# Kernel tuning notes

Measured on AMD Instinct MI355X. Metric: run time of the kernel, lower is better.

Reference implementation:

```python
import jax, jax.numpy as jnp
import numpy as np

NEG_SLOPE = 0.2
EPS = 1e-16


def gat_layer(x, src, dst, W, att_src, att_dst, bias, heads, out_ch, concat, n_nodes):
    # Linear projection -> [N, H, C]
    h = (x @ W).reshape(n_nodes, heads, out_ch)
    # Per-node attention logits [N, H]
    a_src = (h * att_src[None]).sum(-1)
    a_dst = (h * att_dst[None]).sum(-1)
    # Per-edge logits, LeakyReLU (message j -> i with src=j, dst=i)
    alpha = a_src[src] + a_dst[dst]                      # [E, H]
    alpha = jnp.where(alpha >= 0, alpha, NEG_SLOPE * alpha)
    # Segment softmax over incoming edges of each dst node
    amax = jax.ops.segment_max(alpha, dst, num_segments=n_nodes)  # [N, H]
    ealpha = jnp.exp(alpha - amax[dst])
    denom = jax.ops.segment_sum(ealpha, dst, num_segments=n_nodes)
    alpha = ealpha / (denom[dst] + EPS)
    # Weighted messages + scatter-add aggregation
    msg = h[src] * alpha[..., None]                      # [E, H, C]
    out = jax.ops.segment_sum(msg, dst, num_segments=n_nodes)  # [N, H, C]
    out = out.reshape(n_nodes, heads * out_ch) if concat else out.mean(axis=1)
    return out + bias


def setup_inputs() -> dict:
    key = jax.random.key(0)
    ks = jax.random.split(key, 11)
    N, E, F, H, C1 = 50000, 1600000, 128, 8, 8
    x = jax.random.normal(ks[0], (N, F), dtype=jnp.float32)
    edge_index = jax.random.randint(ks[1], (2, E), 0, N, dtype=jnp.int64)
    s = 1.0 / np.sqrt(F)
    W1 = jax.random.normal(ks[2], (F, H * C1), dtype=jnp.float32) * s
    att_src1 = jax.random.normal(ks[3], (H, C1), dtype=jnp.float32) * 0.1
    att_dst1 = jax.random.normal(ks[4], (H, C1), dtype=jnp.float32) * 0.1
    bias1 = jax.random.normal(ks[5], (H * C1,), dtype=jnp.float32) * 0.1
    W2 = jax.random.normal(ks[6], (H * C1, F), dtype=jnp.float32) * (1.0 / np.sqrt(H * C1))
    att_src2 = jax.random.normal(ks[7], (1, F), dtype=jnp.float32) * 0.1
    att_dst2 = jax.random.normal(ks[8], (1, F), dtype=jnp.float32) * 0.1
    bias2 = jax.random.normal(ks[9], (F,), dtype=jnp.float32) * 0.1
    return {"x": x, "edge_index": edge_index, "W1": W1, "att_src1": att_src1,
            "att_dst1": att_dst1, "bias1": bias1, "W2": W2, "att_src2": att_src2,
            "att_dst2": att_dst2, "bias2": bias2}


def reference(x, edge_index, W1, att_src1, att_dst1, bias1, W2, att_src2, att_dst2, bias2):
    N = x.shape[0]
    # PyG GATConv add_self_loops=True: append (i, i) for every node
    loops = jnp.arange(N, dtype=edge_index.dtype)
    src = jnp.concatenate([edge_index[0], loops])
    dst = jnp.concatenate([edge_index[1], loops])
    # eval mode: dropouts are identity
    h = gat_layer(x, src, dst, W1, att_src1, att_dst1, bias1, heads=8, out_ch=8,
                  concat=True, n_nodes=N)            # [N, 64]
    h = jax.nn.elu(h)
    out = gat_layer(h, src, dst, W2, att_src2, att_dst2, bias2, heads=1, out_ch=128,
                    concat=False, n_nodes=N)         # [N, 128]
    return out
```

## Files before the change

### kernel.cpp

```cpp
#include <hip/hip_runtime.h>
#include <stdint.h>

#define NEG_SLOPE 0.2f
#define EPSV 1e-16f
#define NBLK 256

typedef __attribute__((ext_vector_type(8))) short short8;
typedef __attribute__((ext_vector_type(4))) float f32x4;

__device__ inline short bf16r(float f){
  union { float f; unsigned u; } v; v.f = f;
  unsigned r = (v.u + 0x7FFFu + ((v.u >> 16) & 1u)) >> 16;
  return (short)r;
}
__device__ inline float bf16lo(unsigned u){
  union { unsigned u; float f; } v; v.u = u << 16; return v.f;
}
__device__ inline float bf16hi(unsigned u){
  union { unsigned u; float f; } v; v.u = u & 0xFFFF0000u; return v.f;
}

__device__ inline void get_edge(const void* ei, int is64, int E, int e, int& s, int& d){
  if (e >= E){ s = d = e - E; return; }
  if (is64){
    const long long* p = (const long long*)ei;
    s = (int)p[e]; d = (int)p[(long long)E + e];
  } else {
    const int* p = (const int*)ei;
    s = p[e]; d = p[E + e];
  }
}

__device__ inline int get_dst(const void* ei, int is64, int E, int e){
  if (e >= E) return e - E;
  if (is64) return (int)((const long long*)ei)[(long long)E + e];
  return ((const int*)ei)[E + e];
}

__global__ void detect_dtype(const int* ei32, int* flag){
  if (threadIdx.x == 0 && blockIdx.x == 0){
    int nz = 0;
    for (int i = 0; i < 64; ++i) nz |= ei32[2*i + 1];
    *flag = (nz == 0) ? 1 : 0;
  }
}

__global__ void cvt_to_bf16(const float* __restrict__ x, short* __restrict__ xb, int n4){
  int i = blockIdx.x*blockDim.x + threadIdx.x;
  if (i >= n4) return;
  f32x4 v = *(const f32x4*)(x + (size_t)i*4);
  short4 o;
  o.x = bf16r(v[0]); o.y = bf16r(v[1]); o.z = bf16r(v[2]); o.w = bf16r(v[3]);
  *(short4*)(xb + (size_t)i*4) = o;
}

__device__ inline void pack_one(const float* W, short* Wp, int NCOL, int idx){
  int NNT = NCOL >> 4;
  int j = idx & 7, n16 = (idx >> 3) & 15, q = (idx >> 7) & 3, tile = idx >> 9;
  int nt = tile % NNT, kt = tile / NNT;
  int k = kt*32 + q*8 + j, n = nt*16 + n16;
  Wp[idx] = bf16r(W[k*NCOL + n]);
}
__global__ void pack_w_both(const float* __restrict__ W1, short* __restrict__ W1p,
                            const float* __restrict__ W2, short* __restrict__ W2p){
  int idx = blockIdx.x*blockDim.x + threadIdx.x;
  if (idx < 8192) pack_one(W1, W1p, 64, idx);
  else            pack_one(W2, W2p, 128, idx - 8192);
}

template<int K, int NCOL>
__global__ __launch_bounds__(256) void gemm_mfma(const short* __restrict__ A, const short* __restrict__ Bp,
                                                 short* __restrict__ Cb, int M){
  constexpr int NKT = K/32, NNT = NCOL/16;
  int wave = (blockIdx.x*256 + (int)threadIdx.x) >> 6;
  int lane = threadIdx.x & 63;
  int row0 = wave << 4;
  if (row0 >= M) return;
  int m = lane & 15, q = lane >> 4;
  f32x4 acc[NNT];
#pragma unroll
  for (int i = 0; i < NNT; ++i) acc[i] = (f32x4){0.f,0.f,0.f,0.f};
#pragma unroll
  for (int kt = 0; kt < NKT; ++kt){
    short8 a = *(const short8*)(A + (size_t)(row0 + m)*K + kt*32 + q*8);
#pragma unroll
    for (int nt = 0; nt < NNT; ++nt){
      short8 b = *(const short8*)(Bp + (size_t)(((kt*NNT + nt)*4 + q)*16 + m)*8);
      acc[nt] = __builtin_amdgcn_mfma_f32_16x16x32_bf16(a, b, acc[nt], 0, 0, 0);
    }
  }
#pragma unroll
  for (int nt = 0; nt < NNT; ++nt){
#pragma unroll
    for (int r = 0; r < 4; ++r){
      Cb[(size_t)(row0 + q*4 + r)*NCOL + nt*16 + m] = bf16r(acc[nt][r]);
    }
  }
}

__global__ void logits_l1(const unsigned short* __restrict__ h1b, const float* __restrict__ att_s,
                          const float* __restrict__ att_d, float* __restrict__ asrc,
                          float* __restrict__ adst, int N){
  int tid = threadIdx.x;
  int n = blockIdx.x*4 + (tid >> 6);
  int j = tid & 63;
  if (n >= N) return;
  float h = bf16lo((unsigned)h1b[(size_t)n*64 + j]);
  float ps = h * att_s[j];
  float pd = h * att_d[j];
#pragma unroll
  for (int mm = 4; mm; mm >>= 1){ ps += __shfl_xor(ps, mm, 8); pd += __shfl_xor(pd, mm, 8); }
  if ((j & 7) == 0){ asrc[n*8 + (j >> 3)] = ps; adst[n*8 + (j >> 3)] = pd; }
}

__global__ void logits_l2(const unsigned* __restrict__ h2u, const float* __restrict__ att_s,
                          const float* __restrict__ att_d, float* __restrict__ asrc,
                          float* __restrict__ adst, int N){
  int tid = threadIdx.x;
  int n = blockIdx.x*4 + (tid >> 6);
  int l = tid & 63;
  if (n >= N) return;
  unsigned u = h2u[(size_t)n*64 + l];
  float x0 = bf16lo(u), x1 = bf16hi(u);
  float ps = x0*att_s[2*l] + x1*att_s[2*l + 1];
  float pd = x0*att_d[2*l] + x1*att_d[2*l + 1];
#pragma unroll
  for (int mm = 32; mm; mm >>= 1){ ps += __shfl_xor(ps, mm, 64); pd += __shfl_xor(pd, mm, 64); }
  if (l == 0){ asrc[n] = ps; adst[n] = pd; }
}

__global__ __launch_bounds__(256) void p1_hist(const void* ei, const int* flag, int E, int E2,
                                               int* __restrict__ block_counts){
  __shared__ int h[256];
  int t = threadIdx.x, blk = blockIdx.x;
  h[t] = 0; __syncthreads();
  int chunk = (E2 + NBLK - 1)/NBLK;
  int beg = blk*chunk, end = min(beg + chunk, E2);
  int is64 = *flag;
  for (int e = beg + t; e < end; e += 256){
    int d = get_dst(ei, is64, E, e);
    atomicAdd(&h[d >> 8], 1);
  }
  __syncthreads();
  block_counts[blk*256 + t] = h[t];
}

__global__ void p2_bucket_scan(const int* __restrict__ block_counts, int* __restrict__ bucket_base){
  __shared__ int sd[256];
  int t = threadIdx.x;
  int tot = 0;
  for (int b = 0; b < NBLK; ++b) tot += block_counts[b*256 + t];
  sd[t] = tot; __syncthreads();
  for (int off = 1; off < 256; off <<= 1){
    int v = (t >= off) ? sd[t - off] : 0;
    __syncthreads(); sd[t] += v; __syncthreads();
  }
  bucket_base[t] = sd[t] - tot;
  if (t == 255) bucket_base[256] = sd[255];
}

__global__ void p2_block_off(const int* __restrict__ block_counts, const int* __restrict__ bucket_base,
                             int* __restrict__ block_off){
  __shared__ int sd[256];
  int b = blockIdx.x, t = threadIdx.x;
  int v = block_counts[t*256 + b];
  sd[t] = v; __syncthreads();
  for (int off = 1; off < 256; off <<= 1){
    int u = (t >= off) ? sd[t - off] : 0;
    __syncthreads(); sd[t] += u; __syncthreads();
  }
  block_off[t*256 + b] = bucket_base[b] + sd[t] - v;
}

__global__ __launch_bounds__(256) void p3_scatter(const void* ei, const int* flag, int E, int E2,
                                                  const int* __restrict__ block_off,
                                                  unsigned* __restrict__ packed){
  __shared__ int cur[256];
  int t = threadIdx.x, blk = blockIdx.x;
  cur[t] = block_off[blk*256 + t];
  __syncthreads();
  int chunk = (E2 + NBLK - 1)/NBLK;
  int beg = blk*chunk, end = min(beg + chunk, E2);
  int is64 = *flag;
  for (int e = beg + t; e < end; e += 256){
    int s, d; get_edge(ei, is64, E, e, s, d);
    int pos = atomicAdd(&cur[d >> 8], 1);
    packed[pos] = ((unsigned)s << 8) | (unsigned)(d & 255);
  }
}

__global__ __launch_bounds__(256) void p4_sort(const unsigned* __restrict__ packed,
                                               const int* __restrict__ bucket_base,
                                               int N, int E2,
                                               int* __restrict__ offs, int* __restrict__ srcs){
  __shared__ int hist[256];
  __shared__ int cur[256];
  int b = blockIdx.x, t = threadIdx.x;
  int base = bucket_base[b], cnt = bucket_base[b + 1] - base;
  hist[t] = 0; __syncthreads();
  for (int p = t; p < cnt; p += 256){
    atomicAdd(&hist[packed[base + p] & 255u], 1);
  }
  __syncthreads();
  int v = hist[t];
  cur[t] = v; __syncthreads();
  for (int off = 1; off < 256; off <<= 1){
    int u = (t >= off) ? cur[t - off] : 0;
    __syncthreads(); cur[t] += u; __syncthreads();
  }
  int ex = cur[t] - v;
  __syncthreads();
  cur[t] = ex;
  int node = b*256 + t;
  if (node < N) offs[node] = base + ex;
  __syncthreads();
  for (int p = t; p < cnt; p += 256){
    unsigned pk = packed[base + p];
    int pos = atomicAdd(&cur[pk & 255u], 1);
    srcs[base + pos] = (int)(pk >> 8);
  }
  if (b == 0 && t == 0) offs[N] = E2;
}

__global__ __launch_bounds__(256) void agg_l1(const char* __restrict__ h1b,
                       const float* __restrict__ asrc, const float* __restrict__ adst,
                       const int* __restrict__ offs, const int* __restrict__ srcs,
                       const float* __restrict__ bias, uint4* __restrict__ hout, int N){
  int tid = threadIdx.x;
  int i = blockIdx.x*4 + (tid >> 6);
  if (i >= N) return;
  int lane = tid & 63, g = lane >> 3, c = lane & 7;
  float ad = adst[i*8 + c];
  int beg = offs[i], end = offs[i + 1], last = end - 1;
  float acc[8];
#pragma unroll
  for (int k = 0; k < 8; ++k) acc[k] = 0.f;
  float den = 0.f;
  for (int p = beg; p < end; p += 32){
    int m[4], s[4];
#pragma unroll
    for (int k = 0; k < 4; ++k) m[k] = p + 8*k + g;
#pragma unroll
    for (int k = 0; k < 4; ++k) s[k] = srcs[min(m[k], last)];
    float a[4];
#pragma unroll
    for (int k = 0; k < 4; ++k) a[k] = asrc[s[k]*8 + c];
    uint4 v[4];
#pragma unroll
    for (int k = 0; k < 4; ++k) v[k] = *(const uint4*)(h1b + ((size_t)s[k] << 7) + (c << 4));
    float w[4];
#pragma unroll
    for (int k = 0; k < 4; ++k){
      float z = a[k] + ad; z = (z >= 0.f) ? z : NEG_SLOPE*z;
      w[k] = (m[k] < end) ? __expf(z) : 0.f;
      den += w[k];
    }
#pragma unroll
    for (int k = 0; k < 4; ++k){
      acc[0] = fmaf(w[k], bf16lo(v[k].x), acc[0]); acc[1] = fmaf(w[k], bf16hi(v[k].x), acc[1]);
      acc[2] = fmaf(w[k], bf16lo(v[k].y), acc[2]); acc[3] = fmaf(w[k], bf16hi(v[k].y), acc[3]);
      acc[4] = fmaf(w[k], bf16lo(v[k].z), acc[4]); acc[5] = fmaf(w[k], bf16hi(v[k].z), acc[5]);
      acc[6] = fmaf(w[k], bf16lo(v[k].w), acc[6]); acc[7] = fmaf(w[k], bf16hi(v[k].w), acc[7]);
    }
  }
#pragma unroll
  for (int mm = 8; mm <= 32; mm <<= 1){
#pragma unroll
    for (int k = 0; k < 8; ++k) acc[k] += __shfl_xor(acc[k], mm, 64);
    den += __shfl_xor(den, mm, 64);
  }
  if (g == 0){
    float inv = 1.f/(den + EPSV);
    unsigned pk[4];
#pragma unroll
    for (int k = 0; k < 4; ++k){
      float o0 = acc[2*k]*inv     + bias[c*8 + 2*k];
      float o1 = acc[2*k + 1]*inv + bias[c*8 + 2*k + 1];
      o0 = (o0 > 0.f) ? o0 : (__expf(o0) - 1.f);
      o1 = (o1 > 0.f) ? o1 : (__expf(o1) - 1.f);
      pk[k] = (unsigned)(unsigned short)bf16r(o0) | ((unsigned)(unsigned short)bf16r(o1) << 16);
    }
    uint4 o; o.x = pk[0]; o.y = pk[1]; o.z = pk[2]; o.w = pk[3];
    hout[(size_t)i*8 + c] = o;
  }
}

__global__ __launch_bounds__(256) void agg_l2(const char* __restrict__ h2b,
                       const float* __restrict__ asrc, const float* __restrict__ adst,
                       const int* __restrict__ offs, const int* __restrict__ srcs,
                       const float* __restrict__ bias, float* __restrict__ out, int N){
  int tid = threadIdx.x;
  int i = blockIdx.x*4 + (tid >> 6);
  if (i >= N) return;
  int lane = tid & 63, g = lane >> 4, c = lane & 15;
  float ad = adst[i];
  int beg = offs[i], end = offs[i + 1], last = end - 1;
  float acc[8];
#pragma unroll
  for (int k = 0; k < 8; ++k) acc[k] = 0.f;
  float den = 0.f;
  for (int p = beg; p < end; p += 16){
    int m[4], s[4];
#pragma unroll
    for (int k = 0; k < 4; ++k) m[k] = p + 4*k + g;
#pragma unroll
    for (int k = 0; k < 4; ++k) s[k] = srcs[min(m[k], last)];
    float a[4];
#pragma unroll
    for (int k = 0; k < 4; ++k) a[k] = asrc[s[k]];
    uint4 v[4];
#pragma unroll
    for (int k = 0; k < 4; ++k) v[k] = *(const uint4*)(h2b + ((size_t)s[k] << 8) + (c << 4));
    float w[4];
#pragma unroll
    for (int k = 0; k < 4; ++k){
      float z = a[k] + ad; z = (z >= 0.f) ? z : NEG_SLOPE*z;
      w[k] = (m[k] < end) ? __expf(z) : 0.f;
      den += w[k];
    }
#pragma unroll
    for (int k = 0; k < 4; ++k){
      acc[0] = fmaf(w[k], bf16lo(v[k].x), acc[0]); acc[1] = fmaf(w[k], bf16hi(v[k].x), acc[1]);
      acc[2] = fmaf(w[k], bf16lo(v[k].y), acc[2]); acc[3] = fmaf(w[k], bf16hi(v[k].y), acc[3]);
      acc[4] = fmaf(w[k], bf16lo(v[k].z), acc[4]); acc[5] = fmaf(w[k], bf16hi(v[k].z), acc[5]);
      acc[6] = fmaf(w[k], bf16lo(v[k].w), acc[6]); acc[7] = fmaf(w[k], bf16hi(v[k].w), acc[7]);
    }
  }
#pragma unroll
  for (int mm = 16; mm <= 32; mm <<= 1){
#pragma unroll
    for (int k = 0; k < 8; ++k) acc[k] += __shfl_xor(acc[k], mm, 64);
    den += __shfl_xor(den, mm, 64);
  }
  if (g == 0){
    float inv = 1.f/(den + EPSV);
    f32x4 o0, o1;
#pragma unroll
    for (int k = 0; k < 4; ++k) o0[k] = acc[k]*inv     + bias[c*8 + k];
#pragma unroll
    for (int k = 0; k < 4; ++k) o1[k] = acc[4 + k]*inv + bias[c*8 + 4 + k];
    *(f32x4*)(out + (size_t)i*128 + c*8)     = o0;
    *(f32x4*)(out + (size_t)i*128 + c*8 + 4) = o1;
  }
}

extern "C" void kernel_launch(void* const* d_in, const int* in_sizes, int n_in,
                              void* d_out, int out_size, void* d_ws, size_t ws_size,
                              hipStream_t stream){
  const float* x   = (const float*)d_in[0];
  const void*  ei  = d_in[1];
  const float* W1  = (const float*)d_in[2];
  const float* as1 = (const float*)d_in[3];
  const float* ad1 = (const float*)d_in[4];
  const float* b1  = (const float*)d_in[5];
  const float* W2  = (const float*)d_in[6];
  const float* as2 = (const float*)d_in[7];
  const float* ad2 = (const float*)d_in[8];
  const float* b2  = (const float*)d_in[9];

  int N  = in_sizes[0] / 128;
  int E  = in_sizes[1] / 2;
  int E2 = E + N;
  int NB = (N + 255) >> 8;

  char* p = (char*)d_ws;
  auto alloc = [&](size_t bytes) -> void* {
    void* r = (void*)p;
    p += (bytes + 255) & ~(size_t)255;
    return r;
  };
  short*    xb     = (short*)alloc((size_t)N*128*2);
  short*    W1p    = (short*)alloc((size_t)128*64*2);
  short*    W2p    = (short*)alloc((size_t)64*128*2);
  short*    h1b    = (short*)alloc((size_t)N*64*2);
  float*    asrc1  = (float*)alloc((size_t)N*8*4);
  float*    adst1  = (float*)alloc((size_t)N*8*4);
  short*    hin2   = (short*)alloc((size_t)N*64*2);
  short*    h2b    = (short*)alloc((size_t)N*128*2);
  float*    asrc2  = (float*)alloc((size_t)N*4);
  float*    adst2  = (float*)alloc((size_t)N*4);
  int*      offs   = (int*)alloc((size_t)(N + 1)*4);
  int*      srcs   = (int*)alloc((size_t)E2*4);
  unsigned* packed = (unsigned*)alloc((size_t)E2*4);
  int*      bcnt   = (int*)alloc((size_t)NBLK*256*4);
  int*      boff   = (int*)alloc((size_t)NBLK*256*4);
  int*      bbase  = (int*)alloc(257*4);
  int*      flag   = (int*)alloc(4);

  dim3 B(256);
  detect_dtype<<<1, 64, 0, stream>>>((const int*)ei, flag);

  int n4 = N*128/4;
  cvt_to_bf16<<<(n4 + 255)/256, B, 0, stream>>>(x, xb, n4);
  pack_w_both<<<16384/256, B, 0, stream>>>(W1, W1p, W2, W2p);

  int nwav = (N + 15)/16;
  gemm_mfma<128,64><<<(nwav + 3)/4, B, 0, stream>>>(xb, W1p, h1b, N);
  logits_l1<<<(N + 3)/4, B, 0, stream>>>((const unsigned short*)h1b, as1, ad1, asrc1, adst1, N);

  p1_hist<<<NBLK, B, 0, stream>>>(ei, flag, E, E2, bcnt);
  p2_bucket_scan<<<1, B, 0, stream>>>(bcnt, bbase);
  p2_block_off<<<256, B, 0, stream>>>(bcnt, bbase, boff);
  p3_scatter<<<NBLK, B, 0, stream>>>(ei, flag, E, E2, boff, packed);
  p4_sort<<<NB, B, 0, stream>>>(packed, bbase, N, E2, offs, srcs);

  agg_l1<<<(N + 3)/4, B, 0, stream>>>((const char*)h1b, asrc1, adst1, offs, srcs, b1,
                                      (uint4*)hin2, N);

  gemm_mfma<64,128><<<(nwav + 3)/4, B, 0, stream>>>(hin2, W2p, h2b, N);
  logits_l2<<<(N + 3)/4, B, 0, stream>>>((const unsigned*)h2b, as2, ad2, asrc2, adst2, N);
  agg_l2<<<(N + 3)/4, B, 0, stream>>>((const char*)h2b, asrc2, adst2, offs, srcs, b2,
                                      (float*)d_out, N);
}
```

Baseline: 276.3 us.

## Aggregate layer-2 in 64-dim input space before projecting with W2

Uses linearity to reorder layer 2: attention logits come from precomputed W2·att vectors, folded into the agg_l1 epilogue. Aggregation then gathers 64-wide bf16 rows instead of 128-wide projected rows, and the W2 GEMM with bias runs last on the aggregated features. This halves gather traffic in agg_l2 and removes the logits_l2 kernel, but adds a tiny gemv launch and an extra bf16 rounding on the aggregated result.

Result: faster. 254.2 us (-8.0%).

```diff
diff --git a/kernel.cpp b/kernel.cpp
--- a/kernel.cpp
+++ b/kernel.cpp
@@ -66,6 +66,19 @@
   int idx = blockIdx.x*blockDim.x + threadIdx.x;
   if (idx < 8192) pack_one(W1, W1p, 64, idx);
   else            pack_one(W2, W2p, 128, idx - 8192);
+}
+
+__global__ void gemv_att2(const float* __restrict__ W2, const float* __restrict__ as2,
+                          const float* __restrict__ ad2, float* __restrict__ va_s,
+                          float* __restrict__ va_d){
+  int k = threadIdx.x;
+  float s = 0.f, d = 0.f;
+  for (int c = 0; c < 128; ++c){
+    float w = W2[k*128 + c];
+    s = fmaf(w, as2[c], s);
+    d = fmaf(w, ad2[c], d);
+  }
+  va_s[k] = s; va_d[k] = d;
 }
 
 template<int K, int NCOL>
@@ -98,6 +111,38 @@
   }
 }
 
+template<int K, int NCOL>
+__global__ __launch_bounds__(256) void gemm_mfma_bias(const short* __restrict__ A, const short* __restrict__ Bp,
+                                                      const float* __restrict__ bias,
+                                                      float* __restrict__ C, int M){
+  constexpr int NKT = K/32, NNT = NCOL/16;
+  int wave = (blockIdx.x*256 + (int)threadIdx.x) >> 6;
+  int lane = threadIdx.x & 63;
+  int row0 = wave << 4;
+  if (row0 >= M) return;
+  int m = lane & 15, q = lane >> 4;
+  f32x4 acc[NNT];
+#pragma unroll
+  for (int i = 0; i < NNT; ++i) acc[i] = (f32x4){0.f,0.f,0.f,0.f};
+#pragma unroll
+  for (int kt = 0; kt < NKT; ++kt){
+    short8 a = *(const short8*)(A + (size_t)(row0 + m)*K + kt*32 + q*8);
+#pragma unroll
+    for (int nt = 0; nt < NNT; ++nt){
+      short8 b = *(const short8*)(Bp + (size_t)(((kt*NNT + nt)*4 + q)*16 + m)*8);
+      acc[nt] = __builtin_amdgcn_mfma_f32_16x16x32_bf16(a, b, acc[nt], 0, 0, 0);
+    }
+  }
+#pragma unroll
+  for (int nt = 0; nt < NNT; ++nt){
+    float bv = bias[nt*16 + m];
+#pragma unroll
+    for (int r = 0; r < 4; ++r){
+      C[(size_t)(row0 + q*4 + r)*NCOL + nt*16 + m] = acc[nt][r] + bv;
+    }
+  }
+}
+
 __global__ void logits_l1(const unsigned short* __restrict__ h1b, const float* __restrict__ att_s,
                           const float* __restrict__ att_d, float* __restrict__ asrc,
                           float* __restrict__ adst, int N){
@@ -111,22 +156,6 @@
 #pragma unroll
   for (int mm = 4; mm; mm >>= 1){ ps += __shfl_xor(ps, mm, 8); pd += __shfl_xor(pd, mm, 8); }
   if ((j & 7) == 0){ asrc[n*8 + (j >> 3)] = ps; adst[n*8 + (j >> 3)] = pd; }
-}
-
-__global__ void logits_l2(const unsigned* __restrict__ h2u, const float* __restrict__ att_s,
-                          const float* __restrict__ att_d, float* __restrict__ asrc,
-                          float* __restrict__ adst, int N){
-  int tid = threadIdx.x;
-  int n = blockIdx.x*4 + (tid >> 6);
-  int l = tid & 63;
-  if (n >= N) return;
-  unsigned u = h2u[(size_t)n*64 + l];
-  float x0 = bf16lo(u), x1 = bf16hi(u);
-  float ps = x0*att_s[2*l] + x1*att_s[2*l + 1];
-  float pd = x0*att_d[2*l] + x1*att_d[2*l + 1];
-#pragma unroll
-  for (int mm = 32; mm; mm >>= 1){ ps += __shfl_xor(ps, mm, 64); pd += __shfl_xor(pd, mm, 64); }
-  if (l == 0){ asrc[n] = ps; adst[n] = pd; }
 }
 
 __global__ __launch_bounds__(256) void p1_hist(const void* ei, const int* flag, int E, int E2,
@@ -225,7 +254,10 @@
 __global__ __launch_bounds__(256) void agg_l1(const char* __restrict__ h1b,
                        const float* __restrict__ asrc, const float* __restrict__ adst,
                        const int* __restrict__ offs, const int* __restrict__ srcs,
-                       const float* __restrict__ bias, uint4* __restrict__ hout, int N){
+                       const float* __restrict__ bias,
+                       const float* __restrict__ va_s, const float* __restrict__ va_d,
+                       uint4* __restrict__ hout,
+                       float* __restrict__ asrc2, float* __restrict__ adst2, int N){
   int tid = threadIdx.x;
   int i = blockIdx.x*4 + (tid >> 6);
   if (i >= N) return;
@@ -271,38 +303,51 @@
   }
   if (g == 0){
     float inv = 1.f/(den + EPSV);
+    float o[8];
+#pragma unroll
+    for (int k = 0; k < 8; ++k){
+      float t = acc[k]*inv + bias[c*8 + k];
+      o[k] = (t > 0.f) ? t : (__expf(t) - 1.f);
+    }
     unsigned pk[4];
 #pragma unroll
-    for (int k = 0; k < 4; ++k){
-      float o0 = acc[2*k]*inv     + bias[c*8 + 2*k];
-      float o1 = acc[2*k + 1]*inv + bias[c*8 + 2*k + 1];
-      o0 = (o0 > 0.f) ? o0 : (__expf(o0) - 1.f);
-      o1 = (o1 > 0.f) ? o1 : (__expf(o1) - 1.f);
-      pk[k] = (unsigned)(unsigned short)bf16r(o0) | ((unsigned)(unsigned short)bf16r(o1) << 16);
-    }
-    uint4 o; o.x = pk[0]; o.y = pk[1]; o.z = pk[2]; o.w = pk[3];
-    hout[(size_t)i*8 + c] = o;
-  }
-}
-
-__global__ __launch_bounds__(256) void agg_l2(const char* __restrict__ h2b,
+    for (int k = 0; k < 4; ++k)
+      pk[k] = (unsigned)(unsigned short)bf16r(o[2*k]) | ((unsigned)(unsigned short)bf16r(o[2*k+1]) << 16);
+    uint4 ov; ov.x = pk[0]; ov.y = pk[1]; ov.z = pk[2]; ov.w = pk[3];
+    hout[(size_t)i*8 + c] = ov;
+    float ps = 0.f, pd = 0.f;
+#pragma unroll
+    for (int k = 0; k < 8; ++k){
+      ps = fmaf(o[k], va_s[c*8 + k], ps);
+      pd = fmaf(o[k], va_d[c*8 + k], pd);
+    }
+#pragma unroll
+    for (int mm = 1; mm <= 4; mm <<= 1){
+      ps += __shfl_xor(ps, mm, 8);
+      pd += __shfl_xor(pd, mm, 8);
+    }
+    if (c == 0){ asrc2[i] = ps; adst2[i] = pd; }
+  }
+}
+
+__global__ __launch_bounds__(256) void agg_l2(const char* __restrict__ hin2,
                        const float* __restrict__ asrc, const float* __restrict__ adst,
                        const int* __restrict__ offs, const int* __restrict__ srcs,
-                       const float* __restrict__ bias, float* __restrict__ out, int N){
+                       uint4* __restrict__ qout, int N){
   int tid = threadIdx.x;
   int i = blockIdx.x*4 + (tid >> 6);
   if (i >= N) return;
-  int lane = tid & 63, g = lane >> 4, c = lane & 15;
+  int lane = tid & 63, g = lane >> 3, c = lane & 7;
   float ad = adst[i];
   int beg = offs[i], end = offs[i + 1], last = end - 1;
   float acc[8];
 #pragma unroll
   for (int k = 0; k < 8; ++k) acc[k] = 0.f;
   float den = 0.f;
-  for (int p = beg; p < end; p += 16){
+  for (int p = beg; p < end; p += 32){
     int m[4], s[4];
 #pragma unroll
-    for (int k = 0; k < 4; ++k) m[k] = p + 4*k + g;
+    for (int k = 0; k < 4; ++k) m[k] = p + 8*k + g;
 #pragma unroll
     for (int k = 0; k < 4; ++k) s[k] = srcs[min(m[k], last)];
     float a[4];
@@ -310,7 +355,7 @@
     for (int k = 0; k < 4; ++k) a[k] = asrc[s[k]];
     uint4 v[4];
 #pragma unroll
-    for (int k = 0; k < 4; ++k) v[k] = *(const uint4*)(h2b + ((size_t)s[k] << 8) + (c << 4));
+    for (int k = 0; k < 4; ++k) v[k] = *(const uint4*)(hin2 + ((size_t)s[k] << 7) + (c << 4));
     float w[4];
 #pragma unroll
     for (int k = 0; k < 4; ++k){
@@ -327,20 +372,21 @@
     }
   }
 #pragma unroll
-  for (int mm = 16; mm <= 32; mm <<= 1){
+  for (int mm = 8; mm <= 32; mm <<= 1){
 #pragma unroll
     for (int k = 0; k < 8; ++k) acc[k] += __shfl_xor(acc[k], mm, 64);
     den += __shfl_xor(den, mm, 64);
   }
   if (g == 0){
     float inv = 1.f/(den + EPSV);
-    f32x4 o0, o1;
-#pragma unroll
-    for (int k = 0; k < 4; ++k) o0[k] = acc[k]*inv     + bias[c*8 + k];
-#pragma unroll
-    for (int k = 0; k < 4; ++k) o1[k] = acc[4 + k]*inv + bias[c*8 + 4 + k];
-    *(f32x4*)(out + (size_t)i*128 + c*8)     = o0;
-    *(f32x4*)(out + (size_t)i*128 + c*8 + 4) = o1;
+    unsigned pk[4];
+#pragma unroll
+    for (int k = 0; k < 4; ++k){
+      float o0 = acc[2*k]*inv, o1 = acc[2*k + 1]*inv;
+      pk[k] = (unsigned)(unsigned short)bf16r(o0) | ((unsigned)(unsigned short)bf16r(o1) << 16);
+    }
+    uint4 ov; ov.x = pk[0]; ov.y = pk[1]; ov.z = pk[2]; ov.w = pk[3];
+    qout[(size_t)i*8 + c] = ov;
   }
 }
 
@@ -376,9 +422,11 @@
   float*    asrc1  = (float*)alloc((size_t)N*8*4);
   float*    adst1  = (float*)alloc((size_t)N*8*4);
   short*    hin2   = (short*)alloc((size_t)N*64*2);
-  short*    h2b    = (short*)alloc((size_t)N*128*2);
+  short*    hq     = (short*)alloc((size_t)N*64*2);
   float*    asrc2  = (float*)alloc((size_t)N*4);
   float*    adst2  = (float*)alloc((size_t)N*4);
+  float*    va_s2  = (float*)alloc(64*4);
+  float*    va_d2  = (float*)alloc(64*4);
   int*      offs   = (int*)alloc((size_t)(N + 1)*4);
   int*      srcs   = (int*)alloc((size_t)E2*4);
   unsigned* packed = (unsigned*)alloc((size_t)E2*4);
@@ -393,6 +441,7 @@
   int n4 = N*128/4;
   cvt_to_bf16<<<(n4 + 255)/256, B, 0, stream>>>(x, xb, n4);
   pack_w_both<<<16384/256, B, 0, stream>>>(W1, W1p, W2, W2p);
+  gemv_att2<<<1, 64, 0, stream>>>(W2, as2, ad2, va_s2, va_d2);
 
   int nwav = (N + 15)/16;
   gemm_mfma<128,64><<<(nwav + 3)/4, B, 0, stream>>>(xb, W1p, h1b, N);
@@ -405,10 +454,10 @@
   p4_sort<<<NB, B, 0, stream>>>(packed, bbase, N, E2, offs, srcs);
 
   agg_l1<<<(N + 3)/4, B, 0, stream>>>((const char*)h1b, asrc1, adst1, offs, srcs, b1,
-                                      (uint4*)hin2, N);
-
-  gemm_mfma<64,128><<<(nwav + 3)/4, B, 0, stream>>>(hin2, W2p, h2b, N);
-  logits_l2<<<(N + 3)/4, B, 0, stream>>>((const unsigned*)h2b, as2, ad2, asrc2, adst2, N);
-  agg_l2<<<(N + 3)/4, B, 0, stream>>>((const char*)h2b, asrc2, adst2, offs, srcs, b2,
-                                      (float*)d_out, N);
-}
+                                      va_s2, va_d2, (uint4*)hin2, asrc2, adst2, N);
+
+  agg_l2<<<(N + 3)/4, B, 0, stream>>>((const char*)hin2, asrc2, adst2, offs, srcs,
+                                      (uint4*)hq, N);
+
+  gemm_mfma_bias<64,128><<<(nwav + 3)/4, B, 0, stream>>>(hq, W2p, b2, (float*)d_out, N);
+}
```
